# Optimization experiments

Hardware: AMD Instinct MI355X
Metric: run time of the kernel (lower is better)

Reference implementation:

```python
import jax, jax.numpy as jnp
import numpy as np

MARGIN = 0.3
N = 8192
D = 128
NUM_CLASSES = 256

def setup_inputs() -> dict:
    key = jax.random.key(0)
    k1, k2 = jax.random.split(key)
    inputs = jax.random.normal(k1, (N, D), dtype=jnp.float32)
    targets = jax.random.randint(k2, (N,), 0, NUM_CLASSES, dtype=jnp.int64)
    return {"inputs": inputs, "targets": targets}

def reference(inputs, targets):
    n = inputs.shape[0]
    dt = inputs.dtype
    # pairwise euclidean distances: ||xi||^2 + ||xj||^2 - 2 xi.xj, clamped and sqrt'ed
    sq = jnp.sum(inputs * inputs, axis=1)                     # [n]
    d2 = sq[:, None] + sq[None, :] - 2.0 * (inputs @ inputs.T)
    dist = jnp.sqrt(jnp.clip(d2, 1e-12, None))                # [n, n]
    dsq = dist * dist                                         # squared dists used by the loss

    mask = targets[:, None] == targets[None, :]               # same-identity mask [n, n]

    # positives: torch code sorts and drops the smallest (the self-distance ~1e-6)
    pos_d = jnp.where(mask, dist, jnp.inf)
    min_idx = jnp.argmin(pos_d, axis=1)                       # index of dropped element per row
    excl = jnp.arange(n)[None, :] == min_idx[:, None]
    pos_valid = mask & ~excl                                  # remaining positives
    cnt_p = jnp.sum(pos_valid, axis=1).astype(dt)
    sigma_p = jnp.sum(jnp.where(pos_valid, dsq, 0.0), axis=1) / cnt_p
    max_p = jnp.max(jnp.where(pos_valid, dsq, -jnp.inf), axis=1)
    dist_ap = max_p / sigma_p + 0.5 * jnp.log(sigma_p)        # [n]

    # negatives: all different-identity entries
    neg = ~mask
    cnt_n = jnp.sum(neg, axis=1).astype(dt)
    sigma_n = jnp.sum(jnp.where(neg, dsq, 0.0), axis=1) / cnt_n
    min_n = jnp.min(jnp.where(neg, dsq, jnp.inf), axis=1)
    dist_an = min_n / sigma_n + 0.5 * jnp.log(sigma_n)        # [n]

    # MarginRankingLoss with y=1: mean(max(0, -(an - ap) + margin))
    loss = jnp.mean(jnp.maximum(dist_ap - dist_an + MARGIN, 0.0))
    return loss
```

## Files before the change

kernel.cpp:

```cpp
#include <hip/hip_runtime.h>
#include <math.h>


#define NROWS 8192
#define MARGIN_F 0.3f

typedef short bf16x8 __attribute__((ext_vector_type(8)));
typedef float f32x16 __attribute__((ext_vector_type(16)));
union U4B { uint4 u; bf16x8 h; };

__device__ __forceinline__ unsigned short f2bf(float x) {
    unsigned u = __float_as_uint(x);
    return (unsigned short)((u + 0x7fffu + ((u >> 16) & 1u)) >> 16);
}

__global__ __launch_bounds__(256) void histscan_kernel(const int* __restrict__ tgt,
                                                       int* __restrict__ hist,
                                                       int* __restrict__ cstart,
                                                       int* __restrict__ coffset,
                                                       float* __restrict__ S_class,
                                                       int* __restrict__ done) {
    __shared__ int h[256];
    __shared__ int wsum[4];
    int t = threadIdx.x;
    h[t] = 0;
    S_class[t] = 0.0f;
    if (t == 0) *done = 0;
    __syncthreads();
    const int4* t4 = (const int4*)tgt;
    for (int i = t; i < NROWS / 4; i += 256) {
        int4 v = t4[i];
        atomicAdd(&h[v.x], 1);
        atomicAdd(&h[v.y], 1);
        atomicAdd(&h[v.z], 1);
        atomicAdd(&h[v.w], 1);
    }
    __syncthreads();
    int hv = h[t];
    hist[t] = hv;
    int x = hv;
    #pragma unroll
    for (int d = 1; d < 64; d <<= 1) {
        int y = __shfl_up(x, d, 64);
        if ((t & 63) >= d) x += y;
    }
    if ((t & 63) == 63) wsum[t >> 6] = x;
    __syncthreads();
    int off = 0;
    for (int i = 0; i < (t >> 6); ++i) off += wsum[i];
    int excl = off + x - hv;
    cstart[t] = excl;
    coffset[t] = excl;
    if (t == 255) cstart[256] = NROWS;
}

__global__ __launch_bounds__(256) void prep_kernel(const float* __restrict__ X,
                                                   const int* __restrict__ tgt,
                                                   float* __restrict__ sq,
                                                   float* __restrict__ upk,
                                                   unsigned short* __restrict__ Xbf,
                                                   int* __restrict__ coffset,
                                                   float* __restrict__ S_class,
                                                   float* __restrict__ bsum) {
    int tid = threadIdx.x, w = tid >> 6, l = tid & 63;
    int row0 = blockIdx.x * 32 + w * 8;
    float rs = 0.0f;
    #pragma unroll
    for (int i = 0; i < 8; ++i) {
        int r = row0 + i;
        float2 v = ((const float2*)X)[(size_t)r * 64 + l];
        ushort2 h2;
        h2.x = f2bf(v.x);
        h2.y = f2bf(v.y);
        float s = v.x * v.x + v.y * v.y;
        for (int d = 32; d > 0; d >>= 1) s += __shfl_down(s, d, 64);
        int pos = 0;
        if (l == 0) {
            int c = tgt[r];
            pos = atomicAdd(&coffset[c], 1);
            sq[pos] = s;
            rs += s;
            upk[pos] = __uint_as_float((__float_as_uint(0.5f * s) & 0xffffff00u) | (unsigned)c);
            atomicAdd(&S_class[c], s);
        }
        pos = __shfl(pos, 0, 64);
        int g = pos >> 5, rr = pos & 31;
        ((ushort2*)Xbf)[((size_t)(g * 16 + (l >> 2)) * 32 + rr) * 4 + (l & 3)] = h2;
    }
    __shared__ float bs[4];
    if (l == 0) bs[w] = rs;
    __syncthreads();
    if (tid == 0) bsum[blockIdx.x] = bs[0] + bs[1] + bs[2] + bs[3];
}

__global__ __launch_bounds__(256, 2) void dist_kernel(
        const unsigned short* __restrict__ Xbf, const float* __restrict__ upk,
        const int* __restrict__ cstart, float4* __restrict__ partial,
        int ns_mask, int jb_shift, int tiles) {
    __shared__ float4 sm[64 * 4];
    const int tid = threadIdx.x;
    const int w = tid >> 6, l = tid & 63, hl = l >> 5, l31 = l & 31;
    const int bx = blockIdx.x;
    const int slice = bx & ns_mask;
    const int jb = bx >> jb_shift;
    const int col0 = jb * 64;
    const uint4* Xq = (const uint4*)Xbf;

    bf16x8 Bf[2][8];
    #pragma unroll
    for (int ct = 0; ct < 2; ++ct) {
        const uint4* bp = Xq + (size_t)(jb * 2 + ct) * 512 + hl * 32 + l31;
        #pragma unroll
        for (int kk = 0; kk < 8; ++kk) {
            U4B tb; tb.u = bp[kk * 64];
            Bf[ct][kk] = tb.h;
        }
    }
    int tjt[2];
    tjt[0] = __float_as_int(upk[col0 + l31]) & 0xff;
    tjt[1] = __float_as_int(upk[col0 + 32 + l31]) & 0xff;
    const int c_first = __float_as_int(upk[col0]) & 0xff;
    const int c_last  = __float_as_int(upk[col0 + 63]) & 0xff;
    const int U0 = cstart[c_first];
    const int U1 = cstart[c_last + 1];

    float Sa[2] = {0.f, 0.f};
    float Ss[2] = {0.f, 0.f};
    float Mp[2] = {-INFINITY, -INFINITY};
    float Mn[2] = { INFINITY,  INFINITY};
    const int row_base = slice * tiles * 128;

    for (int t = 0; t < tiles; ++t) {
        const int i0 = row_base + t * 128;

        float ur[16];
        const float4* up = (const float4*)(upk + i0 + w * 32 + 4 * hl);
        #pragma unroll
        for (int g = 0; g < 4; ++g) {
            float4 u4 = up[g * 2];
            ur[g * 4 + 0] = u4.x; ur[g * 4 + 1] = u4.y;
            ur[g * 4 + 2] = u4.z; ur[g * 4 + 3] = u4.w;
        }

        const uint4* ap = Xq + ((size_t)(i0 >> 5) + w) * 512 + hl * 32 + l31;
        f32x16 acc[2];
        acc[0] = (f32x16)0.0f;
        acc[1] = (f32x16)0.0f;
        #pragma unroll
        for (int kk = 0; kk < 8; ++kk) {
            U4B a; a.u = ap[kk * 64];
            acc[0] = __builtin_amdgcn_mfma_f32_32x32x16_bf16(a.h, Bf[0][kk], acc[0], 0, 0, 0);
            acc[1] = __builtin_amdgcn_mfma_f32_32x32x16_bf16(a.h, Bf[1][kk], acc[1], 0, 0, 0);
        }

        if (i0 < U1 && i0 + 128 > U0) {
            #pragma unroll
            for (int ct = 0; ct < 2; ++ct) {
                const int tt = tjt[ct];
                #pragma unroll
                for (int r = 0; r < 16; ++r) {
                    float a = acc[ct][r];
                    float v = ur[r] - a;
                    bool same = ((__float_as_int(ur[r]) & 0xff) == tt);
                    Sa[ct] += a;
                    Ss[ct] += same ? a : 0.0f;
                    Mp[ct] = fmaxf(Mp[ct], same ? v : -INFINITY);
                    Mn[ct] = same ? Mn[ct] : fminf(Mn[ct], v);
                }
            }
        } else {
            #pragma unroll
            for (int ct = 0; ct < 2; ++ct) {
                #pragma unroll
                for (int r = 0; r < 16; ++r) {
                    float a = acc[ct][r];
                    Sa[ct] += a;
                    Mn[ct] = fminf(Mn[ct], ur[r] - a);
                }
            }
        }
    }

    #pragma unroll
    for (int ct = 0; ct < 2; ++ct) {
        Sa[ct] += __shfl_xor(Sa[ct], 32, 64);
        Ss[ct] += __shfl_xor(Ss[ct], 32, 64);
        Mp[ct] = fmaxf(Mp[ct], __shfl_xor(Mp[ct], 32, 64));
        Mn[ct] = fminf(Mn[ct], __shfl_xor(Mn[ct], 32, 64));
    }
    if (l < 32) {
        #pragma unroll
        for (int ct = 0; ct < 2; ++ct)
            sm[(ct * 32 + l31) * 4 + w] = make_float4(Sa[ct], Ss[ct], Mp[ct], Mn[ct]);
    }
    __syncthreads();
    if (tid < 64) {
        float4 a = sm[tid * 4 + 0], b = sm[tid * 4 + 1];
        float4 c2 = sm[tid * 4 + 2], d = sm[tid * 4 + 3];
        float4 o;
        o.x = a.x + b.x + c2.x + d.x;
        o.y = a.y + b.y + c2.y + d.y;
        o.z = fmaxf(fmaxf(a.z, b.z), fmaxf(c2.z, d.z));
        o.w = fminf(fminf(a.w, b.w), fminf(c2.w, d.w));
        partial[(size_t)slice * NROWS + col0 + tid] = o;
    }
}

__global__ __launch_bounds__(256) void combine_kernel(
        const float* __restrict__ sq, const float* __restrict__ upk,
        const int* __restrict__ hist, const float* __restrict__ S_class,
        const float* __restrict__ bsum, const float4* __restrict__ partial,
        float* __restrict__ blocksum, int* __restrict__ done,
        float* __restrict__ out, int ns) {
    __shared__ float red[4];
    __shared__ float hs[4];
    __shared__ int lastflag;
    int tid = threadIdx.x, l = tid & 63, w = tid >> 6;

    float b = bsum[tid];
    for (int d = 32; d > 0; d >>= 1) b += __shfl_down(b, d, 64);
    if (l == 0) red[w] = b;
    __syncthreads();
    float S_all = red[0] + red[1] + red[2] + red[3];

    int j = blockIdx.x * 256 + tid;
    float Sa = 0.f, Ss = 0.f, Mp = -INFINITY, Mn = INFINITY;
    for (int s = 0; s < ns; ++s) {
        float4 p = partial[(size_t)s * NROWS + j];
        Sa += p.x; Ss += p.y;
        Mp = fmaxf(Mp, p.z); Mn = fminf(Mn, p.w);
    }
    float sqj = sq[j];
    int c = __float_as_int(upk[j]) & 0xff;
    float cnt = (float)hist[c];
    float sumall = (float)NROWS * sqj + S_all - 2.0f * Sa;
    float sump = cnt * sqj + S_class[c] - 2.0f * Ss;
    float sumn = sumall - sump;
    float sigp = sump / (cnt - 1.0f);
    float sign_ = sumn / ((float)NROWS - cnt);
    float ap = (sqj + 2.0f * Mp) / sigp + 0.5f * __logf(sigp);
    float an = (sqj + 2.0f * Mn) / sign_ + 0.5f * __logf(sign_);
    float h = fmaxf(ap - an + MARGIN_F, 0.0f);
    for (int d = 32; d > 0; d >>= 1) h += __shfl_down(h, d, 64);
    if (l == 0) hs[w] = h;
    __syncthreads();
    if (tid == 0) {
        float tot = hs[0] + hs[1] + hs[2] + hs[3];
        __hip_atomic_store(&blocksum[blockIdx.x], tot,
                           __ATOMIC_RELEASE, __HIP_MEMORY_SCOPE_AGENT);
        int prev = __hip_atomic_fetch_add(done, 1,
                                          __ATOMIC_ACQ_REL, __HIP_MEMORY_SCOPE_AGENT);
        lastflag = (prev == 31) ? 1 : 0;
    }
    __syncthreads();
    if (lastflag) {
        float s2 = 0.0f;
        if (tid < 32)
            s2 = __hip_atomic_load(&blocksum[tid],
                                   __ATOMIC_ACQUIRE, __HIP_MEMORY_SCOPE_AGENT);
        if (tid < 64) {
            for (int d = 32; d > 0; d >>= 1) s2 += __shfl_down(s2, d, 64);
            if (tid == 0) out[0] = s2 * (1.0f / NROWS);
        }
    }
}

extern "C" void kernel_launch(void* const* d_in, const int* in_sizes, int n_in,
                              void* d_out, int out_size, void* d_ws, size_t ws_size,
                              hipStream_t stream) {
    const float* X = (const float*)d_in[0];
    const int* tgt = (const int*)d_in[1];
    float* out = (float*)d_out;

    float* f = (float*)d_ws;
    int*   hist     = (int*)f;
    float* S_class  = f + 256;
    float* bsum     = f + 512;
    float* blocksum = f + 768;
    int*   cstart   = (int*)(f + 800);
    int*   coffset  = (int*)(f + 1088);
    int*   done     = (int*)(f + 1344);
    float* sq       = f + 2048;
    float* upk      = f + 10240;
    unsigned short* Xbf = (unsigned short*)(f + 18432);
    float4* partial = (float4*)(f + 542720);

    int ns = 8;
    while (ns > 2 && ws_size < ((size_t)542720 + (size_t)ns * NROWS * 4) * sizeof(float))
        ns >>= 1;
    int shift = (ns == 8) ? 3 : (ns == 4) ? 2 : 1;
    int tiles = 64 / ns;

    histscan_kernel<<<1, 256, 0, stream>>>(tgt, hist, cstart, coffset, S_class, done);
    prep_kernel<<<256, 256, 0, stream>>>(X, tgt, sq, upk, Xbf, coffset, S_class, bsum);
    dist_kernel<<<128 * ns, 256, 0, stream>>>(Xbf, upk, cstart, partial,
                                              ns - 1, shift, tiles);
    combine_kernel<<<32, 256, 0, stream>>>(sq, upk, hist, S_class, bsum,
                                           partial, blocksum, done, out, ns);
}
```

Baseline: 107.0 us.

## Fold half-norm into MFMA init, drop per-pair sum via column-sum identity

The distance kernel now seeds the MFMA accumulators with the half squared norms and multiplies by a sign-flipped bf16 copy of X, so the accumulator directly holds the half-distance value. The total dot-product sum per column is no longer accumulated per tile. Instead it is computed in the combine kernel as a dot product of each row with a global column-sum vector built during prep. The histogram/scan kernel is merged into prep, and its state is reset with a memset. Launch bounds move to 3 waves per SIMD. In exchange, prep writes a second bf16 copy of X, and the combine kernel does a 128-element dot product per row.

Result: slower. 113.2 us (+5.8%).

```diff
diff --git a/kernel.cpp b/kernel.cpp
--- a/kernel.cpp
+++ b/kernel.cpp
@@ -13,22 +13,33 @@
     unsigned u = __float_as_uint(x);
     return (unsigned short)((u + 0x7fffu + ((u >> 16) & 1u)) >> 16);
 }
-
-__global__ __launch_bounds__(256) void histscan_kernel(const int* __restrict__ tgt,
-                                                       int* __restrict__ hist,
-                                                       int* __restrict__ cstart,
-                                                       int* __restrict__ coffset,
-                                                       float* __restrict__ S_class,
-                                                       int* __restrict__ done) {
+__device__ __forceinline__ float bflo(unsigned u) { return __uint_as_float(u << 16); }
+__device__ __forceinline__ float bfhi(unsigned u) { return __uint_as_float(u & 0xffff0000u); }
+
+__global__ __launch_bounds__(256) void prep_kernel(const float* __restrict__ X,
+                                                   const int* __restrict__ tgt,
+                                                   float* __restrict__ sq,
+                                                   float* __restrict__ upk,
+                                                   unsigned int* __restrict__ Xbf,
+                                                   unsigned int* __restrict__ Xbfn,
+                                                   int* __restrict__ hist,
+                                                   int* __restrict__ ccnt,
+                                                   int* __restrict__ cstart,
+                                                   float* __restrict__ S_class,
+                                                   float* __restrict__ bsum,
+                                                   float* __restrict__ rowsum) {
     __shared__ int h[256];
+    __shared__ int csh[256];
     __shared__ int wsum[4];
-    int t = threadIdx.x;
-    h[t] = 0;
-    S_class[t] = 0.0f;
-    if (t == 0) *done = 0;
+    __shared__ float rsm[4][128];
+    __shared__ float bs[4];
+    int tid = threadIdx.x, w = tid >> 6, l = tid & 63;
+    int bx = blockIdx.x;
+
+    h[tid] = 0;
     __syncthreads();
     const int4* t4 = (const int4*)tgt;
-    for (int i = t; i < NROWS / 4; i += 256) {
+    for (int i = tid; i < NROWS / 4; i += 256) {
         int4 v = t4[i];
         atomicAdd(&h[v.x], 1);
         atomicAdd(&h[v.y], 1);
@@ -36,67 +47,76 @@
         atomicAdd(&h[v.w], 1);
     }
     __syncthreads();
-    int hv = h[t];
-    hist[t] = hv;
+    int hv = h[tid];
     int x = hv;
     #pragma unroll
     for (int d = 1; d < 64; d <<= 1) {
         int y = __shfl_up(x, d, 64);
-        if ((t & 63) >= d) x += y;
-    }
-    if ((t & 63) == 63) wsum[t >> 6] = x;
+        if ((tid & 63) >= d) x += y;
+    }
+    if ((tid & 63) == 63) wsum[tid >> 6] = x;
     __syncthreads();
     int off = 0;
-    for (int i = 0; i < (t >> 6); ++i) off += wsum[i];
+    for (int i = 0; i < (tid >> 6); ++i) off += wsum[i];
     int excl = off + x - hv;
-    cstart[t] = excl;
-    coffset[t] = excl;
-    if (t == 255) cstart[256] = NROWS;
-}
-
-__global__ __launch_bounds__(256) void prep_kernel(const float* __restrict__ X,
-                                                   const int* __restrict__ tgt,
-                                                   float* __restrict__ sq,
-                                                   float* __restrict__ upk,
-                                                   unsigned short* __restrict__ Xbf,
-                                                   int* __restrict__ coffset,
-                                                   float* __restrict__ S_class,
-                                                   float* __restrict__ bsum) {
-    int tid = threadIdx.x, w = tid >> 6, l = tid & 63;
-    int row0 = blockIdx.x * 32 + w * 8;
-    float rs = 0.0f;
+    csh[tid] = excl;
+    if (bx == 0) {
+        hist[tid] = hv;
+        cstart[tid] = excl;
+        if (tid == 255) cstart[256] = NROWS;
+    }
+
+    int row0 = bx * 32 + w * 8;
+    unsigned h2s[8];
+    float s8[8];
+    int c8[8];
+    float rsx = 0.0f, rsy = 0.0f, rs = 0.0f;
     #pragma unroll
     for (int i = 0; i < 8; ++i) {
         int r = row0 + i;
         float2 v = ((const float2*)X)[(size_t)r * 64 + l];
-        ushort2 h2;
-        h2.x = f2bf(v.x);
-        h2.y = f2bf(v.y);
+        unsigned hx = f2bf(v.x), hy = f2bf(v.y);
+        h2s[i] = hx | (hy << 16);
+        rsx += v.x; rsy += v.y;
         float s = v.x * v.x + v.y * v.y;
         for (int d = 32; d > 0; d >>= 1) s += __shfl_down(s, d, 64);
+        if (l == 0) {
+            c8[i] = tgt[r];
+            s8[i] = s;
+            rs += s;
+        }
+    }
+    rsm[w][2 * l] = rsx;
+    rsm[w][2 * l + 1] = rsy;
+    if (l == 0) bs[w] = rs;
+    __syncthreads();
+    if (tid < 128)
+        atomicAdd(&rowsum[tid], rsm[0][tid] + rsm[1][tid] + rsm[2][tid] + rsm[3][tid]);
+    if (tid == 0) bsum[bx] = bs[0] + bs[1] + bs[2] + bs[3];
+
+    #pragma unroll
+    for (int i = 0; i < 8; ++i) {
         int pos = 0;
         if (l == 0) {
-            int c = tgt[r];
-            pos = atomicAdd(&coffset[c], 1);
-            sq[pos] = s;
-            rs += s;
-            upk[pos] = __uint_as_float((__float_as_uint(0.5f * s) & 0xffffff00u) | (unsigned)c);
-            atomicAdd(&S_class[c], s);
+            int c = c8[i];
+            pos = csh[c] + atomicAdd(&ccnt[c], 1);
+            sq[pos] = s8[i];
+            upk[pos] = __uint_as_float((__float_as_uint(0.5f * s8[i]) & 0xffffff00u) | (unsigned)c);
+            atomicAdd(&S_class[c], s8[i]);
         }
         pos = __shfl(pos, 0, 64);
         int g = pos >> 5, rr = pos & 31;
-        ((ushort2*)Xbf)[((size_t)(g * 16 + (l >> 2)) * 32 + rr) * 4 + (l & 3)] = h2;
-    }
-    __shared__ float bs[4];
-    if (l == 0) bs[w] = rs;
-    __syncthreads();
-    if (tid == 0) bsum[blockIdx.x] = bs[0] + bs[1] + bs[2] + bs[3];
-}
-
-__global__ __launch_bounds__(256, 2) void dist_kernel(
-        const unsigned short* __restrict__ Xbf, const float* __restrict__ upk,
-        const int* __restrict__ cstart, float4* __restrict__ partial,
-        int ns_mask, int jb_shift, int tiles) {
+        size_t idx = ((size_t)(g * 16 + (l >> 2)) * 32 + rr) * 4 + (l & 3);
+        unsigned hh = h2s[i];
+        Xbf[idx] = hh;
+        Xbfn[idx] = hh ^ 0x80008000u;
+    }
+}
+
+__global__ __launch_bounds__(256, 3) void dist_kernel(
+        const unsigned short* __restrict__ Xbf, const unsigned short* __restrict__ Xbfn,
+        const float* __restrict__ upk, const int* __restrict__ cstart,
+        float4* __restrict__ partial, int ns_mask, int jb_shift, int tiles) {
     __shared__ float4 sm[64 * 4];
     const int tid = threadIdx.x;
     const int w = tid >> 6, l = tid & 63, hl = l >> 5, l31 = l & 31;
@@ -105,6 +125,7 @@
     const int jb = bx >> jb_shift;
     const int col0 = jb * 64;
     const uint4* Xq = (const uint4*)Xbf;
+    const uint4* Xqn = (const uint4*)Xbfn;
 
     bf16x8 Bf[2][8];
     #pragma unroll
@@ -124,7 +145,6 @@
     const int U0 = cstart[c_first];
     const int U1 = cstart[c_last + 1];
 
-    float Sa[2] = {0.f, 0.f};
     float Ss[2] = {0.f, 0.f};
     float Mp[2] = {-INFINITY, -INFINITY};
     float Mn[2] = { INFINITY,  INFINITY};
@@ -142,10 +162,13 @@
             ur[g * 4 + 2] = u4.z; ur[g * 4 + 3] = u4.w;
         }
 
-        const uint4* ap = Xq + ((size_t)(i0 >> 5) + w) * 512 + hl * 32 + l31;
+        f32x16 ainit;
+        #pragma unroll
+        for (int r = 0; r < 16; ++r) ainit[r] = ur[r];
         f32x16 acc[2];
-        acc[0] = (f32x16)0.0f;
-        acc[1] = (f32x16)0.0f;
+        acc[0] = ainit;
+        acc[1] = ainit;
+        const uint4* ap = Xqn + ((size_t)(i0 >> 5) + w) * 512 + hl * 32 + l31;
         #pragma unroll
         for (int kk = 0; kk < 8; ++kk) {
             U4B a; a.u = ap[kk * 64];
@@ -159,10 +182,9 @@
                 const int tt = tjt[ct];
                 #pragma unroll
                 for (int r = 0; r < 16; ++r) {
-                    float a = acc[ct][r];
-                    float v = ur[r] - a;
+                    float v = acc[ct][r];
                     bool same = ((__float_as_int(ur[r]) & 0xff) == tt);
-                    Sa[ct] += a;
+                    float a = ur[r] - v;
                     Ss[ct] += same ? a : 0.0f;
                     Mp[ct] = fmaxf(Mp[ct], same ? v : -INFINITY);
                     Mn[ct] = same ? Mn[ct] : fminf(Mn[ct], v);
@@ -172,18 +194,14 @@
             #pragma unroll
             for (int ct = 0; ct < 2; ++ct) {
                 #pragma unroll
-                for (int r = 0; r < 16; ++r) {
-                    float a = acc[ct][r];
-                    Sa[ct] += a;
-                    Mn[ct] = fminf(Mn[ct], ur[r] - a);
-                }
+                for (int r = 0; r < 16; r += 2)
+                    Mn[ct] = fminf(fminf(acc[ct][r], acc[ct][r + 1]), Mn[ct]);
             }
         }
     }
 
     #pragma unroll
     for (int ct = 0; ct < 2; ++ct) {
-        Sa[ct] += __shfl_xor(Sa[ct], 32, 64);
         Ss[ct] += __shfl_xor(Ss[ct], 32, 64);
         Mp[ct] = fmaxf(Mp[ct], __shfl_xor(Mp[ct], 32, 64));
         Mn[ct] = fminf(Mn[ct], __shfl_xor(Mn[ct], 32, 64));
@@ -191,7 +209,7 @@
     if (l < 32) {
         #pragma unroll
         for (int ct = 0; ct < 2; ++ct)
-            sm[(ct * 32 + l31) * 4 + w] = make_float4(Sa[ct], Ss[ct], Mp[ct], Mn[ct]);
+            sm[(ct * 32 + l31) * 4 + w] = make_float4(Ss[ct], Mp[ct], Mn[ct], 0.0f);
     }
     __syncthreads();
     if (tid < 64) {
@@ -199,23 +217,28 @@
         float4 c2 = sm[tid * 4 + 2], d = sm[tid * 4 + 3];
         float4 o;
         o.x = a.x + b.x + c2.x + d.x;
-        o.y = a.y + b.y + c2.y + d.y;
-        o.z = fmaxf(fmaxf(a.z, b.z), fmaxf(c2.z, d.z));
-        o.w = fminf(fminf(a.w, b.w), fminf(c2.w, d.w));
+        o.y = fmaxf(fmaxf(a.y, b.y), fmaxf(c2.y, d.y));
+        o.z = fminf(fminf(a.z, b.z), fminf(c2.z, d.z));
+        o.w = 0.0f;
         partial[(size_t)slice * NROWS + col0 + tid] = o;
     }
 }
 
 __global__ __launch_bounds__(256) void combine_kernel(
         const float* __restrict__ sq, const float* __restrict__ upk,
+        const unsigned int* __restrict__ Xbf,
         const int* __restrict__ hist, const float* __restrict__ S_class,
-        const float* __restrict__ bsum, const float4* __restrict__ partial,
+        const float* __restrict__ bsum, const float* __restrict__ rowsum,
+        const float4* __restrict__ partial,
         float* __restrict__ blocksum, int* __restrict__ done,
         float* __restrict__ out, int ns) {
     __shared__ float red[4];
     __shared__ float hs[4];
+    __shared__ float rsl[128];
     __shared__ int lastflag;
     int tid = threadIdx.x, l = tid & 63, w = tid >> 6;
+
+    if (tid < 128) rsl[tid] = rowsum[tid];
 
     float b = bsum[tid];
     for (int d = 32; d > 0; d >>= 1) b += __shfl_down(b, d, 64);
@@ -224,16 +247,36 @@
     float S_all = red[0] + red[1] + red[2] + red[3];
 
     int j = blockIdx.x * 256 + tid;
-    float Sa = 0.f, Ss = 0.f, Mp = -INFINITY, Mn = INFINITY;
+    float Ss = 0.f, Mp = -INFINITY, Mn = INFINITY;
     for (int s = 0; s < ns; ++s) {
         float4 p = partial[(size_t)s * NROWS + j];
-        Sa += p.x; Ss += p.y;
-        Mp = fmaxf(Mp, p.z); Mn = fminf(Mn, p.w);
-    }
+        Ss += p.x;
+        Mp = fmaxf(Mp, p.y); Mn = fminf(Mn, p.z);
+    }
+
+    float sa = 0.0f;
+    {
+        const uint4* Xq = (const uint4*)Xbf;
+        int g = j >> 5, rr = j & 31;
+        #pragma unroll
+        for (int c16 = 0; c16 < 16; ++c16) {
+            uint4 q = Xq[((size_t)(g * 16 + c16)) * 32 + rr];
+            int k0 = c16 * 8;
+            sa = fmaf(bflo(q.x), rsl[k0 + 0], sa);
+            sa = fmaf(bfhi(q.x), rsl[k0 + 1], sa);
+            sa = fmaf(bflo(q.y), rsl[k0 + 2], sa);
+            sa = fmaf(bfhi(q.y), rsl[k0 + 3], sa);
+            sa = fmaf(bflo(q.z), rsl[k0 + 4], sa);
+            sa = fmaf(bfhi(q.z), rsl[k0 + 5], sa);
+            sa = fmaf(bflo(q.w), rsl[k0 + 6], sa);
+            sa = fmaf(bfhi(q.w), rsl[k0 + 7], sa);
+        }
+    }
+
     float sqj = sq[j];
     int c = __float_as_int(upk[j]) & 0xff;
     float cnt = (float)hist[c];
-    float sumall = (float)NROWS * sqj + S_all - 2.0f * Sa;
+    float sumall = (float)NROWS * sqj + S_all - 2.0f * sa;
     float sump = cnt * sqj + S_class[c] - 2.0f * Ss;
     float sumn = sumall - sump;
     float sigp = sump / (cnt - 1.0f);
@@ -275,26 +318,31 @@
     float* f = (float*)d_ws;
     int*   hist     = (int*)f;
     float* S_class  = f + 256;
-    float* bsum     = f + 512;
-    float* blocksum = f + 768;
-    int*   cstart   = (int*)(f + 800);
-    int*   coffset  = (int*)(f + 1088);
-    int*   done     = (int*)(f + 1344);
+    int*   ccnt     = (int*)(f + 512);
+    float* rowsum   = f + 768;
+    int*   done     = (int*)(f + 897);
+    float* bsum     = f + 1024;
+    float* blocksum = f + 1280;
+    int*   cstart   = (int*)(f + 1536);
     float* sq       = f + 2048;
     float* upk      = f + 10240;
-    unsigned short* Xbf = (unsigned short*)(f + 18432);
-    float4* partial = (float4*)(f + 542720);
+    unsigned int* Xbf  = (unsigned int*)(f + 18432);
+    unsigned int* Xbfn = (unsigned int*)(f + 542720);
+    float4* partial = (float4*)(f + 1067008);
 
     int ns = 8;
-    while (ns > 2 && ws_size < ((size_t)542720 + (size_t)ns * NROWS * 4) * sizeof(float))
+    while (ns > 2 && ws_size < ((size_t)1067008 + (size_t)ns * NROWS * 4) * sizeof(float))
         ns >>= 1;
     int shift = (ns == 8) ? 3 : (ns == 4) ? 2 : 1;
     int tiles = 64 / ns;
 
-    histscan_kernel<<<1, 256, 0, stream>>>(tgt, hist, cstart, coffset, S_class, done);
-    prep_kernel<<<256, 256, 0, stream>>>(X, tgt, sq, upk, Xbf, coffset, S_class, bsum);
-    dist_kernel<<<128 * ns, 256, 0, stream>>>(Xbf, upk, cstart, partial,
+    hipMemsetAsync(d_ws, 0, 3600, stream);
+    prep_kernel<<<256, 256, 0, stream>>>(X, tgt, sq, upk, Xbf, Xbfn,
+                                         hist, ccnt, cstart, S_class, bsum, rowsum);
+    dist_kernel<<<128 * ns, 256, 0, stream>>>((const unsigned short*)Xbf,
+                                              (const unsigned short*)Xbfn,
+                                              upk, cstart, partial,
                                               ns - 1, shift, tiles);
-    combine_kernel<<<32, 256, 0, stream>>>(sq, upk, hist, S_class, bsum,
-                                           partial, blocksum, done, out, ns);
-}
+    combine_kernel<<<32, 256, 0, stream>>>(sq, upk, Xbf, hist, S_class, bsum,
+                                           rowsum, partial, blocksum, done, out, ns);
+}
```
